# Kernel tuning notes

Measured on AMD Instinct MI355X. Metric: run time of the kernel, lower is better.

Reference implementation:

```python
import jax, jax.numpy as jnp
import numpy as np

MIN_EXP = 1    # log2(min_window=2)
MAX_EXP = 10   # log2(max_window=1024)
OUT_LEN = 16384  # reconstructed signal length L; encoded len = L*(1 - 2**-MAX_EXP)


def setup_inputs() -> dict:
    key = jax.random.key(0)
    k1, k2, k3 = jax.random.split(key, 3)
    B = 2048
    enc_len = OUT_LEN * (2 ** (1 - MIN_EXP)) - OUT_LEN // (2 ** MAX_EXP)  # 16368
    weights_len = 2 * (2 ** MAX_EXP) - 1  # 2047
    stdev = 1.0 / np.sqrt(weights_len)
    data = jax.random.normal(k1, (B, enc_len), dtype=jnp.float32)
    weights = jax.random.uniform(k2, (weights_len,), dtype=jnp.float32, minval=-stdev, maxval=stdev)
    bias = jax.random.uniform(k3, (MAX_EXP,), dtype=jnp.float32, minval=-stdev, maxval=stdev)
    return {"data": data, "weights": weights, "bias": bias}


def reference(data, weights, bias):
    """Transposed time-scale convolution: for each dyadic scale e (window w=2**e),
    the shared kernel weights[w-1:2w-1] is overlap-added (stride == window, so the
    windows tile the output exactly) scaled by that scale's coefficients, summed
    across scales, with a per-scale bias."""
    B = data.shape[0]
    out = jnp.zeros((B, OUT_LEN), dtype=data.dtype)
    offset = 0
    for e in range(MIN_EXP, MAX_EXP + 1):
        w = 2 ** e
        n = OUT_LEN // w                      # number of windows at this scale
        kern = weights[w - 1: 2 * w - 1]      # [w] kernel for this scale
        coeffs = data[:, offset: offset + n]  # [B, n]
        offset += n
        # transposed conv with stride = kernel size: outer product then tile
        contrib = (coeffs[:, :, None] * kern[None, None, :]).reshape(B, OUT_LEN)
        out = out + contrib + bias[e - 1]
    return out
```

## Files before the change

kernel.cpp:

```cpp
#include <hip/hip_runtime.h>
#include <hip/hip_bf16.h>

#define TSC_OUT_LEN 16384
#define TSC_ENC_LEN 16368

__global__ __launch_bounds__(256) void tsc_transpose_kernel(
    const float* __restrict__ data,
    const float* __restrict__ weights,
    const float* __restrict__ bias,
    float* __restrict__ out)
{
    __shared__ float wl[2048];
    const int tid = threadIdx.x;
    for (int i = tid; i < 2047; i += 256) wl[i + 1] = weights[i];
    if (tid == 0) wl[0] = 0.0f;
    __syncthreads();

    float bs = 0.0f;
#pragma unroll
    for (int i = 0; i < 10; ++i) bs += bias[i];

    const int b    = blockIdx.x >> 3;
    const int tile = (blockIdx.x & 7) << 11;
    const int j0   = tile + (tid << 3);
    const float* drow = data + (size_t)b * TSC_ENC_LEN;

    float acc[8];
#pragma unroll
    for (int k = 0; k < 8; ++k) acc[k] = bs;

    {
        const float4 d4 = *reinterpret_cast<const float4*>(drow + (j0 >> 1));
        const float w1 = wl[2], w2 = wl[3];
        acc[0] += d4.x * w1; acc[1] += d4.x * w2;
        acc[2] += d4.y * w1; acc[3] += d4.y * w2;
        acc[4] += d4.z * w1; acc[5] += d4.z * w2;
        acc[6] += d4.w * w1; acc[7] += d4.w * w2;
    }
    {
        const float2 d2 = *reinterpret_cast<const float2*>(drow + 8192 + (j0 >> 2));
        const float4 kv = *reinterpret_cast<const float4*>(&wl[4]);
        acc[0] += d2.x * kv.x; acc[1] += d2.x * kv.y;
        acc[2] += d2.x * kv.z; acc[3] += d2.x * kv.w;
        acc[4] += d2.y * kv.x; acc[5] += d2.y * kv.y;
        acc[6] += d2.y * kv.z; acc[7] += d2.y * kv.w;
    }
#pragma unroll
    for (int e = 3; e <= 10; ++e) {
        const int w   = 1 << e;
        const int off = TSC_OUT_LEN - (TSC_OUT_LEN >> (e - 1));
        const float c = drow[off + (j0 >> e)];
        const int  kb = w + (j0 & (w - 1));
        const float4 k0 = *reinterpret_cast<const float4*>(&wl[kb]);
        const float4 k1 = *reinterpret_cast<const float4*>(&wl[kb + 4]);
        acc[0] += c * k0.x; acc[1] += c * k0.y;
        acc[2] += c * k0.z; acc[3] += c * k0.w;
        acc[4] += c * k1.x; acc[5] += c * k1.y;
        acc[6] += c * k1.z; acc[7] += c * k1.w;
    }

    float4* o = reinterpret_cast<float4*>(out + (size_t)b * TSC_OUT_LEN + j0);
    o[0] = make_float4(acc[0], acc[1], acc[2], acc[3]);
    o[1] = make_float4(acc[4], acc[5], acc[6], acc[7]);
}

extern "C" void kernel_launch(void* const* d_in, const int* in_sizes, int n_in,
                              void* d_out, int out_size, void* d_ws, size_t ws_size,
                              hipStream_t stream) {
    const float* data    = (const float*)d_in[0];
    const float* weights = (const float*)d_in[1];
    const float* bias    = (const float*)d_in[2];
    float* out = (float*)d_out;

    const int B = in_sizes[0] / TSC_ENC_LEN;
    dim3 grid(B * 8);
    dim3 block(256);
    tsc_transpose_kernel<<<grid, block, 0, stream>>>(data, weights, bias, out);
}
```

Baseline: 238.9 us.

## Process two rows per block with double-buffered LDS staging of coarse coefficients

```diff
diff --git a/kernel.cpp b/kernel.cpp
--- a/kernel.cpp
+++ b/kernel.cpp
@@ -1,8 +1,14 @@
 #include <hip/hip_runtime.h>
-#include <hip/hip_bf16.h>
 
 #define TSC_OUT_LEN 16384
 #define TSC_ENC_LEN 16368
+
+#define TSC_WAIT8() asm volatile("s_waitcnt vmcnt(8)" ::: "memory")
+#define TSC_BAR() do { __builtin_amdgcn_s_barrier(); asm volatile("" ::: "memory"); } while (0)
+
+__device__ __forceinline__ float tsc_rfl(float x) {
+    return __uint_as_float(__builtin_amdgcn_readfirstlane(__float_as_uint(x)));
+}
 
 __global__ __launch_bounds__(256) void tsc_transpose_kernel(
     const float* __restrict__ data,
@@ -11,57 +17,157 @@
     float* __restrict__ out)
 {
     __shared__ float wl[2048];
+    __shared__ __align__(16) float dL[2][4096];
+
     const int tid = threadIdx.x;
     for (int i = tid; i < 2047; i += 256) wl[i + 1] = weights[i];
-    if (tid == 0) wl[0] = 0.0f;
     __syncthreads();
+
+    const int lane = tid & 63;
+    const int wu   = __builtin_amdgcn_readfirstlane(tid >> 6);
+    int off0[4], offh[4], ldsb[4]; bool val[4];
+#pragma unroll
+    for (int k = 0; k < 4; ++k) {
+        const int cid = k + (wu << 2);
+        const int s   = lane + (cid << 6);
+        int e, base;
+        if      (s < 512)  { e = 2;  base = 0;    }
+        else if (s < 768)  { e = 3;  base = 512;  }
+        else if (s < 896)  { e = 4;  base = 768;  }
+        else if (s < 960)  { e = 5;  base = 896;  }
+        else if (s < 992)  { e = 6;  base = 960;  }
+        else if (s < 1008) { e = 7;  base = 992;  }
+        else if (s < 1016) { e = 8;  base = 1008; }
+        else if (s < 1020) { e = 9;  base = 1016; }
+        else               { e = 10; base = 1020; }
+        off0[k] = TSC_OUT_LEN - (32768 >> e) + ((s - base) << 2);
+        offh[k] = 1 << (13 - e);
+        ldsb[k] = cid << 8;
+        val[k]  = (s < 1022);
+    }
 
     float bs = 0.0f;
 #pragma unroll
     for (int i = 0; i < 10; ++i) bs += bias[i];
 
-    const int b    = blockIdx.x >> 3;
-    const int tile = (blockIdx.x & 7) << 11;
-    const int j0   = tile + (tid << 3);
-    const float* drow = data + (size_t)b * TSC_ENC_LEN;
+    const float w1a = tsc_rfl(wl[2]), w1b = tsc_rfl(wl[3]);
+    const float w2a = tsc_rfl(wl[4]), w2b = tsc_rfl(wl[5]);
+    const float w2c = tsc_rfl(wl[6]), w2d = tsc_rfl(wl[7]);
+    float w3[8];
+#pragma unroll
+    for (int i = 0; i < 8; ++i) w3[i] = tsc_rfl(wl[8 + i]);
 
-    float acc[8];
+    const int j8 = tid << 3;
+    int kbA[7];
 #pragma unroll
-    for (int k = 0; k < 8; ++k) acc[k] = bs;
-
-    {
-        const float4 d4 = *reinterpret_cast<const float4*>(drow + (j0 >> 1));
-        const float w1 = wl[2], w2 = wl[3];
-        acc[0] += d4.x * w1; acc[1] += d4.x * w2;
-        acc[2] += d4.y * w1; acc[3] += d4.y * w2;
-        acc[4] += d4.z * w1; acc[5] += d4.z * w2;
-        acc[6] += d4.w * w1; acc[7] += d4.w * w2;
-    }
-    {
-        const float2 d2 = *reinterpret_cast<const float2*>(drow + 8192 + (j0 >> 2));
-        const float4 kv = *reinterpret_cast<const float4*>(&wl[4]);
-        acc[0] += d2.x * kv.x; acc[1] += d2.x * kv.y;
-        acc[2] += d2.x * kv.z; acc[3] += d2.x * kv.w;
-        acc[4] += d2.y * kv.x; acc[5] += d2.y * kv.y;
-        acc[6] += d2.y * kv.z; acc[7] += d2.y * kv.w;
-    }
-#pragma unroll
-    for (int e = 3; e <= 10; ++e) {
-        const int w   = 1 << e;
-        const int off = TSC_OUT_LEN - (TSC_OUT_LEN >> (e - 1));
-        const float c = drow[off + (j0 >> e)];
-        const int  kb = w + (j0 & (w - 1));
-        const float4 k0 = *reinterpret_cast<const float4*>(&wl[kb]);
-        const float4 k1 = *reinterpret_cast<const float4*>(&wl[kb + 4]);
-        acc[0] += c * k0.x; acc[1] += c * k0.y;
-        acc[2] += c * k0.z; acc[3] += c * k0.w;
-        acc[4] += c * k1.x; acc[5] += c * k1.y;
-        acc[6] += c * k1.z; acc[7] += c * k1.w;
+    for (int e = 4; e <= 10; ++e) {
+        const int w = 1 << e;
+        kbA[e - 4] = w + (j8 & (w - 1));
     }
 
-    float4* o = reinterpret_cast<float4*>(out + (size_t)b * TSC_OUT_LEN + j0);
-    o[0] = make_float4(acc[0], acc[1], acc[2], acc[3]);
-    o[1] = make_float4(acc[4], acc[5], acc[6], acc[7]);
+    const int b0 = blockIdx.x << 1;
+    const float* dr0 = data + (size_t)b0 * TSC_ENC_LEN;
+    const float* dr1 = dr0 + TSC_ENC_LEN;
+
+    auto dma = [&](const float* dr, int hf, float* buf) {
+#pragma unroll
+        for (int k = 0; k < 4; ++k) {
+            const float* gs = val[k] ? (dr + off0[k] + (hf ? offh[k] : 0)) : dr;
+            __builtin_amdgcn_global_load_lds(
+                (const __attribute__((address_space(1))) unsigned int*)gs,
+                (__attribute__((address_space(3))) unsigned int*)(buf + ldsb[k]),
+                16, 0, 0);
+        }
+    };
+
+#define TSC_LDE1(DR, HF, CA, CB, CC, CD) do {                               \
+        const float* p1_ = (DR) + ((HF) << 12) + (tid << 2);                \
+        CA = *reinterpret_cast<const float4*>(p1_);                         \
+        CB = *reinterpret_cast<const float4*>(p1_ + 1024);                  \
+        CC = *reinterpret_cast<const float4*>(p1_ + 2048);                  \
+        CD = *reinterpret_cast<const float4*>(p1_ + 3072);                  \
+    } while (0)
+
+#define TSC_ITER(DLB, IT, C1, OROW) do {                                    \
+        const int jl = ((IT) << 11) + j8;                                   \
+        const float2 c2 = *reinterpret_cast<const float2*>(&(DLB)[jl >> 2]);\
+        const float c3  = (DLB)[2048 + (jl >> 3)];                          \
+        const float c4  = (DLB)[3072 + (jl >> 4)];                          \
+        const float c5  = (DLB)[3584 + (jl >> 5)];                          \
+        const float c6  = (DLB)[3840 + (jl >> 6)];                          \
+        const float c7  = (DLB)[3968 + (jl >> 7)];                          \
+        const float c8  = (DLB)[4032 + (jl >> 8)];                          \
+        const float c9  = (DLB)[4064 + (jl >> 9)];                          \
+        const float c10 = (DLB)[4080 + (jl >> 10)];                         \
+        float a0 = bs, a1 = bs, a2 = bs, a3 = bs;                           \
+        float a4 = bs, a5 = bs, a6 = bs, a7 = bs;                           \
+        a0 = fmaf((C1).x, w1a, a0); a1 = fmaf((C1).x, w1b, a1);             \
+        a2 = fmaf((C1).y, w1a, a2); a3 = fmaf((C1).y, w1b, a3);             \
+        a4 = fmaf((C1).z, w1a, a4); a5 = fmaf((C1).z, w1b, a5);             \
+        a6 = fmaf((C1).w, w1a, a6); a7 = fmaf((C1).w, w1b, a7);             \
+        a0 = fmaf(c2.x, w2a, a0); a1 = fmaf(c2.x, w2b, a1);                 \
+        a2 = fmaf(c2.x, w2c, a2); a3 = fmaf(c2.x, w2d, a3);                 \
+        a4 = fmaf(c2.y, w2a, a4); a5 = fmaf(c2.y, w2b, a5);                 \
+        a6 = fmaf(c2.y, w2c, a6); a7 = fmaf(c2.y, w2d, a7);                 \
+        a0 = fmaf(c3, w3[0], a0); a1 = fmaf(c3, w3[1], a1);                 \
+        a2 = fmaf(c3, w3[2], a2); a3 = fmaf(c3, w3[3], a3);                 \
+        a4 = fmaf(c3, w3[4], a4); a5 = fmaf(c3, w3[5], a5);                 \
+        a6 = fmaf(c3, w3[6], a6); a7 = fmaf(c3, w3[7], a7);                 \
+        _Pragma("unroll")                                                   \
+        for (int e_ = 4; e_ <= 10; ++e_) {                                  \
+            const int   i_ = e_ - 4;                                        \
+            const float c_ = (i_ == 0) ? c4 : (i_ == 1) ? c5 :              \
+                             (i_ == 2) ? c6 : (i_ == 3) ? c7 :              \
+                             (i_ == 4) ? c8 : (i_ == 5) ? c9 : c10;         \
+            const float4 k0 = *reinterpret_cast<const float4*>(&wl[kbA[i_]]);   \
+            const float4 k1 = *reinterpret_cast<const float4*>(&wl[kbA[i_] + 4]);\
+            a0 = fmaf(c_, k0.x, a0); a1 = fmaf(c_, k0.y, a1);               \
+            a2 = fmaf(c_, k0.z, a2); a3 = fmaf(c_, k0.w, a3);               \
+            a4 = fmaf(c_, k1.x, a4); a5 = fmaf(c_, k1.y, a5);               \
+            a6 = fmaf(c_, k1.z, a6); a7 = fmaf(c_, k1.w, a7);               \
+        }                                                                   \
+        float4* o4 = reinterpret_cast<float4*>((OROW) + ((IT) << 11));      \
+        o4[0] = make_float4(a0, a1, a2, a3);                                \
+        o4[1] = make_float4(a4, a5, a6, a7);                                \
+    } while (0)
+
+#define TSC_COMPUTE(DLB, CA, CB, CC, CD, OROW) do {                         \
+        TSC_ITER(DLB, 0, CA, OROW);                                         \
+        TSC_ITER(DLB, 1, CB, OROW);                                         \
+        TSC_ITER(DLB, 2, CC, OROW);                                         \
+        TSC_ITER(DLB, 3, CD, OROW);                                         \
+    } while (0)
+
+    float4 A0, A1, A2, A3;
+    float4 B0, B1, B2, B3;
+
+    dma(dr0, 0, dL[0]);  TSC_LDE1(dr0, 0, A0, A1, A2, A3);
+    dma(dr0, 1, dL[1]);  TSC_LDE1(dr0, 1, B0, B1, B2, B3);
+
+    float* o0 = out + (size_t)b0 * TSC_OUT_LEN + j8;
+    float* o1 = o0 + TSC_OUT_LEN;
+
+    TSC_WAIT8();
+    TSC_BAR();
+    TSC_COMPUTE(dL[0], A0, A1, A2, A3, o0);
+
+    TSC_WAIT8();
+    TSC_BAR();
+    dma(dr1, 0, dL[0]);  TSC_LDE1(dr1, 0, A0, A1, A2, A3);
+    TSC_COMPUTE(dL[1], B0, B1, B2, B3, o0 + 8192);
+
+    TSC_WAIT8();
+    TSC_BAR();
+    dma(dr1, 1, dL[1]);  TSC_LDE1(dr1, 1, B0, B1, B2, B3);
+    TSC_COMPUTE(dL[0], A0, A1, A2, A3, o1);
+
+    TSC_WAIT8();
+    TSC_BAR();
+    TSC_COMPUTE(dL[1], B0, B1, B2, B3, o1 + 8192);
+
+#undef TSC_COMPUTE
+#undef TSC_ITER
+#undef TSC_LDE1
 }
 
 extern "C" void kernel_launch(void* const* d_in, const int* in_sizes, int n_in,
@@ -73,7 +179,7 @@
     float* out = (float*)d_out;
 
     const int B = in_sizes[0] / TSC_ENC_LEN;
-    dim3 grid(B * 8);
+    dim3 grid(B / 2);
     dim3 block(256);
     tsc_transpose_kernel<<<grid, block, 0, stream>>>(data, weights, bias, out);
 }
```

Measured after the change: 243.1 us. About the same (+1.8%).
